# Kernel optimization log

Hardware: AMD Instinct MI355X
Metric: run time of the kernel (lower is better)

Reference implementation:

```python
import jax, jax.numpy as jnp
import numpy as np
import math

B, S, D, H = 2, 2048, 2048, 16
HD = D // H  # 128
EPS = 1e-5


def setup_inputs() -> dict:
    key = jax.random.key(0)
    ks = jax.random.split(key, 8)
    s = 0.02
    return {
        "x": jax.random.normal(ks[0], (B, S, D), jnp.float32),
        "ln1_s": jnp.ones((D,), jnp.float32),
        "ln1_b": jnp.zeros((D,), jnp.float32),
        "Wq": jax.random.normal(ks[1], (D, D), jnp.float32) * s,
        "Wk": jax.random.normal(ks[2], (D, D), jnp.float32) * s,
        "Wv": jax.random.normal(ks[3], (D, D), jnp.float32) * s,
        "Wo": jax.random.normal(ks[4], (D, D), jnp.float32) * s,
        "bo": jnp.zeros((D,), jnp.float32),
        "ln2_s": jnp.ones((D,), jnp.float32),
        "ln2_b": jnp.zeros((D,), jnp.float32),
        "W1": jax.random.normal(ks[5], (D, 4 * D), jnp.float32) * s,
        "b1": jnp.zeros((4 * D,), jnp.float32),
        "W2": jax.random.normal(ks[6], (4 * D, D), jnp.float32) * s,
        "b2": jnp.zeros((D,), jnp.float32),
    }


def _layernorm(x, scale, shift):
    mean = jnp.mean(x, axis=-1, keepdims=True)
    var = jnp.var(x, axis=-1, keepdims=True)  # unbiased=False
    return scale * (x - mean) * jax.lax.rsqrt(var + EPS) + shift


def _gelu_tanh(x):
    c = math.sqrt(2.0 / math.pi)
    return 0.5 * x * (1.0 + jnp.tanh(c * (x + 0.044715 * x * x * x)))


def reference(x, ln1_s, ln1_b, Wq, Wk, Wv, Wo, bo, ln2_s, ln2_b, W1, b1, W2, b2):
    b, n, d = x.shape
    # --- pre-norm MHA ---
    xn = _layernorm(x, ln1_s, ln1_b)
    q = (xn @ Wq).reshape(b, n, H, HD)
    k = (xn @ Wk).reshape(b, n, H, HD)
    v = (xn @ Wv).reshape(b, n, H, HD)
    scores = jnp.einsum("bqhd,bkhd->bhqk", q, k) / math.sqrt(HD)
    causal = jnp.tril(jnp.ones((n, n), bool))  # True = keep
    scores = jnp.where(causal, scores, -jnp.inf)
    attn = jax.nn.softmax(scores, axis=-1)
    ctx = jnp.einsum("bhqk,bkhd->bqhd", attn, v).reshape(b, n, d)
    attn_out = ctx @ Wo + bo
    x = x + attn_out
    # --- pre-norm FFN ---
    xn2 = _layernorm(x, ln2_s, ln2_b)
    h = _gelu_tanh(xn2 @ W1 + b1)
    ff_out = h @ W2 + b2
    return x + ff_out
```

## Files before the change

kernel.cpp:

```cpp
#include <hip/hip_runtime.h>

typedef unsigned short u16;
typedef __attribute__((ext_vector_type(8))) short short8;
typedef __attribute__((ext_vector_type(8))) __bf16 bf16x8;
typedef __attribute__((ext_vector_type(4))) float f32x4;

#define DEV __device__ __forceinline__

DEV float bf2f(u16 u) {
    union { unsigned v; float f; } x; x.v = ((unsigned)u) << 16; return x.f;
}
DEV u16 f2bf(float f) {
    union { float f; unsigned v; } x; x.f = f;
    unsigned r = x.v + 0x7fff + ((x.v >> 16) & 1);
    return (u16)(r >> 16);
}

DEV f32x4 mfma16(short8 a, short8 b, f32x4 c) {
    return __builtin_amdgcn_mfma_f32_16x16x32_bf16(
        __builtin_bit_cast(bf16x8, a), __builtin_bit_cast(bf16x8, b), c, 0, 0, 0);
}

typedef const __attribute__((address_space(1))) void* gas_ptr;
typedef __attribute__((address_space(3))) void* las_ptr;

__global__ __launch_bounds__(256) void transpose_kernel(
    const float* __restrict__ in, u16* __restrict__ out, int R, int C)
{
    __shared__ u16 t[64][65];
    int tid = threadIdx.x;
    int bc = blockIdx.x * 64, br = blockIdx.y * 64;
    int r = tid >> 2, cs = (tid & 3) * 16;
    const float* ip = in + (size_t)(br + r) * C + bc + cs;
    f32x4 v0 = *(const f32x4*)ip, v1 = *(const f32x4*)(ip + 4),
          v2 = *(const f32x4*)(ip + 8), v3 = *(const f32x4*)(ip + 12);
#pragma unroll
    for (int j = 0; j < 4; j++) {
        t[r][cs + j]      = f2bf(v0[j]);
        t[r][cs + 4 + j]  = f2bf(v1[j]);
        t[r][cs + 8 + j]  = f2bf(v2[j]);
        t[r][cs + 12 + j] = f2bf(v3[j]);
    }
    __syncthreads();
    int n = tid >> 2, ks = (tid & 3) * 16;
    short8 o0, o1;
#pragma unroll
    for (int j = 0; j < 8; j++) { o0[j] = (short)t[ks + j][n]; o1[j] = (short)t[ks + 8 + j][n]; }
    u16* op = out + (size_t)(bc + n) * R + br + ks;
    *(short8*)op = o0;
    *(short8*)(op + 8) = o1;
}

template<int INBF>
__global__ __launch_bounds__(256) void ln_kernel(
    const void* __restrict__ xp, const float* __restrict__ sc, const float* __restrict__ sh,
    u16* __restrict__ out)
{
    int row = blockIdx.x, tid = threadIdx.x;
    float f[8], sum = 0.f, ss = 0.f;
    if (INBF) {
        short8 v = *(const short8*)((const u16*)xp + (size_t)row * 2048 + tid * 8);
#pragma unroll
        for (int j = 0; j < 8; j++) f[j] = bf2f((u16)v[j]);
    } else {
        const f32x4* xr = (const f32x4*)((const float*)xp + (size_t)row * 2048 + tid * 8);
        f32x4 a = xr[0], b = xr[1];
#pragma unroll
        for (int j = 0; j < 4; j++) { f[j] = a[j]; f[4 + j] = b[j]; }
    }
#pragma unroll
    for (int j = 0; j < 8; j++) { sum += f[j]; ss += f[j] * f[j]; }
#pragma unroll
    for (int m = 1; m < 64; m <<= 1) { sum += __shfl_xor(sum, m, 64); ss += __shfl_xor(ss, m, 64); }
    __shared__ float red[8];
    int w = tid >> 6, l = tid & 63;
    if (l == 0) { red[w] = sum; red[4 + w] = ss; }
    __syncthreads();
    sum = red[0] + red[1] + red[2] + red[3];
    ss  = red[4] + red[5] + red[6] + red[7];
    float mean = sum * (1.f / 2048.f);
    float var  = ss * (1.f / 2048.f) - mean * mean;
    float rstd = rsqrtf(var + 1e-5f);
    const f32x4* sp = (const f32x4*)(sc + tid * 8);
    const f32x4* bp = (const f32x4*)(sh + tid * 8);
    f32x4 s0 = sp[0], s1 = sp[1], b0 = bp[0], b1 = bp[1];
    short8 o;
#pragma unroll
    for (int j = 0; j < 4; j++) {
        o[j]     = (short)f2bf((f[j] - mean) * rstd * s0[j] + b0[j]);
        o[4 + j] = (short)f2bf((f[4 + j] - mean) * rstd * s1[j] + b1[j]);
    }
    *(short8*)(out + (size_t)row * 2048 + tid * 8) = o;
}

template<int EPI, int OUTF, int RESBF, int SPLITM, int SHAREB>
__global__ __launch_bounds__(256, 2) void gemm_bt2(
    const u16* __restrict__ A, const u16* __restrict__ BT, void* __restrict__ Cp,
    const float* __restrict__ bias, const void* __restrict__ res, int M, int N, int K)
{
    __shared__ u16 As[2][128 * 64];
    __shared__ u16 Bs[2][128 * 64];
    int tid = threadIdx.x, l = tid & 63, w = tid >> 6;

    int nbx = gridDim.x, nby = gridDim.y;
    int nwg = nbx * nby;
    int orig = blockIdx.y * nbx + blockIdx.x;
    int nch = nwg >> 3;
    int wg = (orig & 7) * nch + (orig >> 3);
    int bx, by;
    if (SHAREB) { bx = wg / nby; by = wg % nby; }
    else        { by = wg / nbx; bx = wg % nbx; }

    int mbase = by * 128, nbase = bx * 128;
    const u16* Ag = A + (size_t)mbase * K;
    const u16* Bg = BT + (size_t)nbase * K;
    int NT = K >> 6;

    auto stage = [&](const u16* G, u16* Ld, int t) {
#pragma unroll
        for (int g = 0; g < 4; g++) {
            int ci = g * 256 + tid;
            int r = ci >> 3, chp = ci & 7;
            int ch = chp ^ (r & 7);
            const u16* gp = G + (size_t)r * K + t * 64 + ch * 8;
            __builtin_amdgcn_global_load_lds((gas_ptr)gp, (las_ptr)(Ld + (g * 256 + w * 64) * 8), 16, 0, 0);
        }
    };

    f32x4 acc[4][4];
#pragma unroll
    for (int i = 0; i < 4; i++)
#pragma unroll
        for (int j = 0; j < 4; j++) acc[i][j] = (f32x4){0.f, 0.f, 0.f, 0.f};
    int wr = (w >> 1) * 64, wc = (w & 1) * 64;

    stage(Ag, As[0], 0); stage(Bg, Bs[0], 0);
    __syncthreads();
    int buf = 0;
    for (int t = 0; t < NT; ++t) {
        if (t + 1 < NT) { stage(Ag, As[buf ^ 1], t + 1); stage(Bg, Bs[buf ^ 1], t + 1); }
        short8 af[2][4], bfr[2][4];
#pragma unroll
        for (int ks = 0; ks < 2; ks++) {
            int c = ks * 4 + (l >> 4);
#pragma unroll
            for (int i = 0; i < 4; i++) {
                int ra = wr + i * 16 + (l & 15);
                af[ks][i] = *(const short8*)&As[buf][ra * 64 + ((c ^ (ra & 7)) << 3)];
                int rb = wc + i * 16 + (l & 15);
                bfr[ks][i] = *(const short8*)&Bs[buf][rb * 64 + ((c ^ (rb & 7)) << 3)];
            }
        }
        __builtin_amdgcn_s_setprio(1);
#pragma unroll
        for (int ks = 0; ks < 2; ks++)
#pragma unroll
            for (int mi = 0; mi < 4; mi++)
#pragma unroll
                for (int ni = 0; ni < 4; ni++)
                    acc[mi][ni] = mfma16(af[ks][mi], bfr[ks][ni], acc[mi][ni]);
        __builtin_amdgcn_s_setprio(0);
        __syncthreads();
        buf ^= 1;
    }

#pragma unroll
    for (int mi = 0; mi < 4; mi++) {
#pragma unroll
        for (int ni = 0; ni < 4; ni++) {
            int col = nbase + wc + ni * 16 + (l & 15);
            float bval = (EPI != 0) ? bias[col] : 0.f;
#pragma unroll
            for (int r = 0; r < 4; r++) {
                int row = mbase + wr + mi * 16 + (l >> 4) * 4 + r;
                float v = acc[mi][ni][r];
                if (EPI == 1) {
                    size_t ridx = (size_t)row * N + col;
                    float rv = RESBF ? bf2f(((const u16*)res)[ridx]) : ((const float*)res)[ridx];
                    v += bval + rv;
                }
                if (EPI == 2) {
                    v += bval;
                    float tt = tanhf(0.7978845608028654f * (v + 0.044715f * v * v * v));
                    v = 0.5f * v * (1.f + tt);
                }
                if (SPLITM == 1) {
                    ((u16*)Cp)[(size_t)(col >> 11) * 8388608ULL + (size_t)row * 2048 + (col & 2047)] = f2bf(v);
                } else if (SPLITM == 2) {
                    ((u16*)Cp)[(size_t)(col >> 11) * 4194304ULL + (size_t)row * 2048 + (col & 2047)] = f2bf(v);
                } else if (OUTF) {
                    ((float*)Cp)[(size_t)row * N + col] = v;
                } else {
                    ((u16*)Cp)[(size_t)row * N + col] = f2bf(v);
                }
            }
        }
    }
}

__global__ __launch_bounds__(256, 2) void attn_kernel(
    const u16* __restrict__ Q, const u16* __restrict__ Kp, const u16* __restrict__ VTg,
    u16* __restrict__ O)
{
    __shared__ u16 Ks[64 * 128];
    __shared__ u16 VT[128 * 64];
    __shared__ u16 Ps[4 * 2048];
    int tid = threadIdx.x, l = tid & 63, w = tid >> 6;
    int qtl = (int)gridDim.x - 1 - (int)blockIdx.x;
    int bh = blockIdx.y, b = bh >> 4, h = bh & 15;
    const float SCALE = 0.08838834764831845f;
    int qbase = qtl * 128;
    size_t bS = (size_t)b * 2048;
    const u16* vrow = VTg + (size_t)bh * 128 * 2048;

    short8 qf[2][4];
#pragma unroll
    for (int mg = 0; mg < 2; mg++) {
        int qrow = qbase + w * 32 + mg * 16 + (l & 15);
        const u16* qp = Q + (bS + qrow) * 2048 + h * 128 + (l >> 4) * 8;
#pragma unroll
        for (int ds = 0; ds < 4; ds++) qf[mg][ds] = *(const short8*)(qp + ds * 32);
    }
    float m_[2][4], l_[2][4];
    f32x4 o_[2][8];
#pragma unroll
    for (int mg = 0; mg < 2; mg++)
#pragma unroll
        for (int r = 0; r < 4; r++) { m_[mg][r] = -1e30f; l_[mg][r] = 0.f; }
#pragma unroll
    for (int mg = 0; mg < 2; mg++)
#pragma unroll
        for (int d = 0; d < 8; d++) o_[mg][d] = (f32x4){0.f, 0.f, 0.f, 0.f};

    int ktmax = 2 * qtl + 1;
    for (int kt = 0; kt <= ktmax; ++kt) {
        int kbase = kt * 64;
#pragma unroll
        for (int it = 0; it < 4; ++it) {
            int slot = it * 256 + tid;
            int key = slot >> 4, dseg = slot & 15;
            short8 kv = *(const short8*)(Kp + (bS + kbase + key) * 2048 + h * 128 + dseg * 8);
            int kidx = ((key * 256 + dseg * 16) ^ ((key & 7) << 4)) >> 1;
            *(short8*)&Ks[kidx] = kv;
            int d = slot >> 3, k8 = slot & 7;
            short8 vv = *(const short8*)(vrow + (size_t)d * 2048 + kbase + k8 * 8);
            int vidx = ((d * 128 + k8 * 16) ^ ((d & 7) << 4)) >> 1;
            *(short8*)&VT[vidx] = vv;
        }
        __syncthreads();

        f32x4 s[2][4];
#pragma unroll
        for (int mg = 0; mg < 2; mg++)
#pragma unroll
            for (int kg = 0; kg < 4; kg++) s[mg][kg] = (f32x4){0.f, 0.f, 0.f, 0.f};
        __builtin_amdgcn_s_setprio(1);
#pragma unroll
        for (int kg = 0; kg < 4; kg++) {
            int key0 = kg * 16 + (l & 15);
#pragma unroll
            for (int ds = 0; ds < 4; ds++) {
                int i0 = ((key0 * 256 + ds * 64 + (l >> 4) * 16) ^ ((key0 & 7) << 4)) >> 1;
                short8 kb = *(const short8*)&Ks[i0];
                s[0][kg] = mfma16(qf[0][ds], kb, s[0][kg]);
                s[1][kg] = mfma16(qf[1][ds], kb, s[1][kg]);
            }
        }
        __builtin_amdgcn_s_setprio(0);

        bool domask = (kbase + 63) > qbase;
        float alpha[2][4];
        u16* Pw = &Ps[w * 2048];
#pragma unroll
        for (int mg = 0; mg < 2; mg++) {
#pragma unroll
            for (int r = 0; r < 4; r++) {
                int qrow = qbase + w * 32 + mg * 16 + (l >> 4) * 4 + r;
                float aa[4];
#pragma unroll
                for (int kg = 0; kg < 4; kg++) {
                    float a = s[mg][kg][r] * SCALE;
                    if (domask && (kbase + kg * 16 + (l & 15)) > qrow) a = -1e30f;
                    aa[kg] = a;
                }
                float mx = fmaxf(fmaxf(aa[0], aa[1]), fmaxf(aa[2], aa[3]));
                mx = fmaxf(mx, __shfl_xor(mx, 1, 64));
                mx = fmaxf(mx, __shfl_xor(mx, 2, 64));
                mx = fmaxf(mx, __shfl_xor(mx, 4, 64));
                mx = fmaxf(mx, __shfl_xor(mx, 8, 64));
                float mn = fmaxf(m_[mg][r], mx);
                float al = __expf(m_[mg][r] - mn);
                m_[mg][r] = mn;
                float p[4], rs = 0.f;
#pragma unroll
                for (int kg = 0; kg < 4; kg++) { p[kg] = __expf(aa[kg] - mn); rs += p[kg]; }
                rs += __shfl_xor(rs, 1, 64);
                rs += __shfl_xor(rs, 2, 64);
                rs += __shfl_xor(rs, 4, 64);
                rs += __shfl_xor(rs, 8, 64);
                l_[mg][r] = l_[mg][r] * al + rs;
                alpha[mg][r] = al;
#pragma unroll
                for (int kg = 0; kg < 4; kg++) {
                    int col = kg * 16 + (l & 15);
                    int lp = ((l >> 4) * 4 + r) | (((col >> 3) & 3) << 4);
                    Pw[(mg * 2 + (col >> 5)) * 512 + lp * 8 + (col & 7)] = f2bf(p[kg]);
                }
            }
        }
#pragma unroll
        for (int mg = 0; mg < 2; mg++)
#pragma unroll
            for (int dblk = 0; dblk < 8; dblk++)
#pragma unroll
                for (int r = 0; r < 4; r++) o_[mg][dblk][r] *= alpha[mg][r];

        __builtin_amdgcn_s_setprio(1);
#pragma unroll
        for (int kk = 0; kk < 2; kk++) {
            short8 pa0 = *(const short8*)&Pw[(0 * 2 + kk) * 512 + l * 8];
            short8 pa1 = *(const short8*)&Pw[(1 * 2 + kk) * 512 + l * 8];
#pragma unroll
            for (int dblk = 0; dblk < 8; dblk++) {
                int d = dblk * 16 + (l & 15);
                int iv = ((d * 128 + kk * 64 + (l >> 4) * 16) ^ ((d & 7) << 4)) >> 1;
                short8 vb = *(const short8*)&VT[iv];
                o_[0][dblk] = mfma16(pa0, vb, o_[0][dblk]);
                o_[1][dblk] = mfma16(pa1, vb, o_[1][dblk]);
            }
        }
        __builtin_amdgcn_s_setprio(0);
        __syncthreads();
    }

#pragma unroll
    for (int mg = 0; mg < 2; mg++) {
#pragma unroll
        for (int dblk = 0; dblk < 8; dblk++) {
#pragma unroll
            for (int r = 0; r < 4; r++) {
                int qrow = qbase + w * 32 + mg * 16 + (l >> 4) * 4 + r;
                float v = o_[mg][dblk][r] / l_[mg][r];
                O[(bS + qrow) * 2048 + h * 128 + dblk * 16 + (l & 15)] = f2bf(v);
            }
        }
    }
}

extern "C" void kernel_launch(void* const* d_in, const int* in_sizes, int n_in,
                              void* d_out, int out_size, void* d_ws, size_t ws_size,
                              hipStream_t stream)
{
    const float* x    = (const float*)d_in[0];
    const float* ln1s = (const float*)d_in[1];
    const float* ln1b = (const float*)d_in[2];
    const float* Wq   = (const float*)d_in[3];
    const float* Wk   = (const float*)d_in[4];
    const float* Wv   = (const float*)d_in[5];
    const float* Wo   = (const float*)d_in[6];
    const float* bo   = (const float*)d_in[7];
    const float* ln2s = (const float*)d_in[8];
    const float* ln2b = (const float*)d_in[9];
    const float* W1   = (const float*)d_in[10];
    const float* b1   = (const float*)d_in[11];
    const float* W2   = (const float*)d_in[12];
    const float* b2   = (const float*)d_in[13];
    float* out = (float*)d_out;
    const size_t ACT = 8388608ULL;

    u16* ws16 = (u16*)d_ws;
    u16* xn   = ws16;
    u16* q    = ws16 + ACT;
    u16* k    = ws16 + 2 * ACT;
    u16* vT   = ws16 + 3 * ACT;
    u16* hbuf = ws16 + 2 * ACT;
    u16* wt   = ws16 + 6 * ACT;
    u16* x2   = q;
    (void)k;

    dim3 blk(256);
    transpose_kernel<<<dim3(32, 32), blk, 0, stream>>>(Wq, wt,                  2048, 2048);
    transpose_kernel<<<dim3(32, 32), blk, 0, stream>>>(Wk, wt + (ACT >> 1),     2048, 2048);
    transpose_kernel<<<dim3(32, 32), blk, 0, stream>>>(Wv, wt + ACT,            2048, 2048);
    transpose_kernel<<<dim3(32, 32), blk, 0, stream>>>(Wo, wt + 3 * (ACT >> 1), 2048, 2048);
    ln_kernel<0><<<4096, blk, 0, stream>>>(x, ln1s, ln1b, xn);
    gemm_bt2<0, 0, 0, 1, 1><<<dim3(32, 32), blk, 0, stream>>>(xn, wt, q, nullptr, nullptr, 4096, 4096, 2048);
    gemm_bt2<0, 0, 0, 2, 1><<<dim3(32, 16), blk, 0, stream>>>(wt + ACT, xn, vT, nullptr, nullptr, 2048, 4096, 2048);
    attn_kernel<<<dim3(16, 32), blk, 0, stream>>>(q, k, vT, xn);
    gemm_bt2<1, 0, 0, 0, 0><<<dim3(16, 32), blk, 0, stream>>>(xn, wt + 3 * (ACT >> 1), x2, bo, x, 4096, 2048, 2048);
    transpose_kernel<<<dim3(128, 32), blk, 0, stream>>>(W1, wt, 2048, 8192);
    ln_kernel<1><<<4096, blk, 0, stream>>>(x2, ln2s, ln2b, xn);
    gemm_bt2<2, 0, 0, 0, 1><<<dim3(64, 32), blk, 0, stream>>>(xn, wt, hbuf, b1, nullptr, 4096, 8192, 2048);
    transpose_kernel<<<dim3(32, 128), blk, 0, stream>>>(W2, wt, 8192, 2048);
    gemm_bt2<1, 1, 1, 0, 0><<<dim3(16, 32), blk, 0, stream>>>(hbuf, wt, out, b2, x2, 4096, 2048, 8192);
}
```

Before: 669.9 us.

## Replace GEMM with 256x256-tile 8-wave ping-pong pipelined kernel

Replaces the 128x128-tile, 4-wave double-buffered GEMM with a 256x256-tile, 512-thread kernel. Each K step is split into four quarter-tile MFMA phases, and the LDS loads for future K steps are interleaved between phases using explicit barriers, sched_barriers and waitcnts. The larger tile raises arithmetic intensity and the finer staging is meant to overlap global loads with MFMA work. The cost is one workgroup per CU, fewer workgroups per GEMM (e.g. 128 for the 2048-wide outputs) and therefore possible wave-quantization losses, plus fragile hand-written synchronization.

```diff
diff --git a/kernel.cpp b/kernel.cpp
--- a/kernel.cpp
+++ b/kernel.cpp
@@ -6,6 +6,7 @@
 typedef __attribute__((ext_vector_type(4))) float f32x4;
 
 #define DEV __device__ __forceinline__
+#define SB() __builtin_amdgcn_sched_barrier(0)
 
 DEV float bf2f(u16 u) {
     union { unsigned v; float f; } x; x.v = ((unsigned)u) << 16; return x.f;
@@ -94,86 +95,153 @@
 }
 
 template<int EPI, int OUTF, int RESBF, int SPLITM, int SHAREB>
-__global__ __launch_bounds__(256, 2) void gemm_bt2(
+__global__ __launch_bounds__(512, 1) void gemm8p(
     const u16* __restrict__ A, const u16* __restrict__ BT, void* __restrict__ Cp,
     const float* __restrict__ bias, const void* __restrict__ res, int M, int N, int K)
 {
-    __shared__ u16 As[2][128 * 64];
-    __shared__ u16 Bs[2][128 * 64];
+    __shared__ u16 As[2][2][128 * 64];
+    __shared__ u16 Bs[2][2][128 * 64];
     int tid = threadIdx.x, l = tid & 63, w = tid >> 6;
+    int wm = w >> 2, wn = w & 3;
 
     int nbx = gridDim.x, nby = gridDim.y;
     int nwg = nbx * nby;
     int orig = blockIdx.y * nbx + blockIdx.x;
-    int nch = nwg >> 3;
-    int wg = (orig & 7) * nch + (orig >> 3);
+    int wg = (orig & 7) * (nwg >> 3) + (orig >> 3);
     int bx, by;
     if (SHAREB) { bx = wg / nby; by = wg % nby; }
     else        { by = wg / nbx; bx = wg % nbx; }
 
-    int mbase = by * 128, nbase = bx * 128;
+    int mbase = by * 256, nbase = bx * 256;
     const u16* Ag = A + (size_t)mbase * K;
     const u16* Bg = BT + (size_t)nbase * K;
     int NT = K >> 6;
 
-    auto stage = [&](const u16* G, u16* Ld, int t) {
-#pragma unroll
-        for (int g = 0; g < 4; g++) {
-            int ci = g * 256 + tid;
-            int r = ci >> 3, chp = ci & 7;
-            int ch = chp ^ (r & 7);
-            const u16* gp = G + (size_t)r * K + t * 64 + ch * 8;
-            __builtin_amdgcn_global_load_lds((gas_ptr)gp, (las_ptr)(Ld + (g * 256 + w * 64) * 8), 16, 0, 0);
+    auto stageA = [&](int b, int h, int tt) {
+#pragma unroll
+        for (int g = 0; g < 2; g++) {
+            int ci = g * 512 + tid;
+            int pr = ci >> 3, chp = ci & 7;
+            int ch = chp ^ (pr & 7);
+            int gr = (pr & 63) + ((pr >> 6) << 7) + h * 64;
+            const u16* gp = Ag + (size_t)gr * K + tt * 64 + ch * 8;
+            __builtin_amdgcn_global_load_lds((gas_ptr)gp,
+                (las_ptr)&As[b][h][(g * 512 + w * 64) * 8], 16, 0, 0);
         }
     };
-
-    f32x4 acc[4][4];
-#pragma unroll
-    for (int i = 0; i < 4; i++)
+    auto stageB = [&](int b, int h, int tt) {
+#pragma unroll
+        for (int g = 0; g < 2; g++) {
+            int ci = g * 512 + tid;
+            int pr = ci >> 3, chp = ci & 7;
+            int ch = chp ^ (pr & 7);
+            int gr = ((pr >> 5) << 6) + (pr & 31) + h * 32;
+            const u16* gp = Bg + (size_t)gr * K + tt * 64 + ch * 8;
+            __builtin_amdgcn_global_load_lds((gas_ptr)gp,
+                (las_ptr)&Bs[b][h][(g * 512 + w * 64) * 8], 16, 0, 0);
+        }
+    };
+    auto readA = [&](int b, int h, int i, int ks) -> short8 {
+        int pr = wm * 64 + i * 16 + (l & 15);
+        int c = (ks * 4 + (l >> 4)) ^ (pr & 7);
+        return *(const short8*)&As[b][h][pr * 64 + c * 8];
+    };
+    auto readB = [&](int b, int h, int j, int ks) -> short8 {
+        int pr = wn * 32 + j * 16 + (l & 15);
+        int c = (ks * 4 + (l >> 4)) ^ (pr & 7);
+        return *(const short8*)&Bs[b][h][pr * 64 + c * 8];
+    };
+
+    f32x4 acc[8][4];
+#pragma unroll
+    for (int i = 0; i < 8; i++)
 #pragma unroll
         for (int j = 0; j < 4; j++) acc[i][j] = (f32x4){0.f, 0.f, 0.f, 0.f};
-    int wr = (w >> 1) * 64, wc = (w & 1) * 64;
-
-    stage(Ag, As[0], 0); stage(Bg, Bs[0], 0);
-    __syncthreads();
-    int buf = 0;
+
+    stageA(0, 0, 0); stageB(0, 0, 0); stageB(0, 1, 0); stageA(0, 1, 0);
+    stageA(1, 0, 1); stageB(1, 1, 1); stageA(1, 1, 1);
+    asm volatile("s_waitcnt vmcnt(6)" ::: "memory");
+    SB(); __builtin_amdgcn_s_barrier(); SB();
+
     for (int t = 0; t < NT; ++t) {
-        if (t + 1 < NT) { stage(Ag, As[buf ^ 1], t + 1); stage(Bg, Bs[buf ^ 1], t + 1); }
-        short8 af[2][4], bfr[2][4];
-#pragma unroll
-        for (int ks = 0; ks < 2; ks++) {
-            int c = ks * 4 + (l >> 4);
-#pragma unroll
-            for (int i = 0; i < 4; i++) {
-                int ra = wr + i * 16 + (l & 15);
-                af[ks][i] = *(const short8*)&As[buf][ra * 64 + ((c ^ (ra & 7)) << 3)];
-                int rb = wc + i * 16 + (l & 15);
-                bfr[ks][i] = *(const short8*)&Bs[buf][rb * 64 + ((c ^ (rb & 7)) << 3)];
-            }
-        }
+        int p = t & 1, q = p ^ 1;
+        short8 a[4][2], bb[2][2];
+#pragma unroll
+        for (int i = 0; i < 4; i++) { a[i][0] = readA(p, 0, i, 0); a[i][1] = readA(p, 0, i, 1); }
+#pragma unroll
+        for (int j = 0; j < 2; j++) { bb[j][0] = readB(p, 0, j, 0); bb[j][1] = readB(p, 0, j, 1); }
+        if (t + 1 < NT) stageB(q, 0, t + 1);
+        SB(); __builtin_amdgcn_s_barrier();
+        asm volatile("s_waitcnt lgkmcnt(0)" ::: "memory"); SB();
         __builtin_amdgcn_s_setprio(1);
 #pragma unroll
         for (int ks = 0; ks < 2; ks++)
 #pragma unroll
-            for (int mi = 0; mi < 4; mi++)
-#pragma unroll
-                for (int ni = 0; ni < 4; ni++)
-                    acc[mi][ni] = mfma16(af[ks][mi], bfr[ks][ni], acc[mi][ni]);
-        __builtin_amdgcn_s_setprio(0);
-        __syncthreads();
-        buf ^= 1;
-    }
-
-#pragma unroll
-    for (int mi = 0; mi < 4; mi++) {
-#pragma unroll
-        for (int ni = 0; ni < 4; ni++) {
-            int col = nbase + wc + ni * 16 + (l & 15);
+            for (int i = 0; i < 4; i++)
+#pragma unroll
+                for (int j = 0; j < 2; j++)
+                    acc[i][j] = mfma16(a[i][ks], bb[j][ks], acc[i][j]);
+        __builtin_amdgcn_s_setprio(0);
+        SB(); __builtin_amdgcn_s_barrier(); SB();
+#pragma unroll
+        for (int j = 0; j < 2; j++) { bb[j][0] = readB(p, 1, j, 0); bb[j][1] = readB(p, 1, j, 1); }
+        if (t + 2 < NT) stageA(p, 0, t + 2);
+        SB(); __builtin_amdgcn_s_barrier();
+        asm volatile("s_waitcnt lgkmcnt(0)" ::: "memory"); SB();
+        __builtin_amdgcn_s_setprio(1);
+#pragma unroll
+        for (int ks = 0; ks < 2; ks++)
+#pragma unroll
+            for (int i = 0; i < 4; i++)
+#pragma unroll
+                for (int j = 0; j < 2; j++)
+                    acc[i][2 + j] = mfma16(a[i][ks], bb[j][ks], acc[i][2 + j]);
+        __builtin_amdgcn_s_setprio(0);
+        SB(); __builtin_amdgcn_s_barrier(); SB();
+#pragma unroll
+        for (int i = 0; i < 4; i++) { a[i][0] = readA(p, 1, i, 0); a[i][1] = readA(p, 1, i, 1); }
+        if (t + 2 < NT) stageB(p, 1, t + 2);
+        SB(); __builtin_amdgcn_s_barrier();
+        asm volatile("s_waitcnt lgkmcnt(0)" ::: "memory"); SB();
+        __builtin_amdgcn_s_setprio(1);
+#pragma unroll
+        for (int ks = 0; ks < 2; ks++)
+#pragma unroll
+            for (int i = 0; i < 4; i++)
+#pragma unroll
+                for (int j = 0; j < 2; j++)
+                    acc[4 + i][2 + j] = mfma16(a[i][ks], bb[j][ks], acc[4 + i][2 + j]);
+        __builtin_amdgcn_s_setprio(0);
+        SB(); __builtin_amdgcn_s_barrier(); SB();
+#pragma unroll
+        for (int j = 0; j < 2; j++) { bb[j][0] = readB(p, 0, j, 0); bb[j][1] = readB(p, 0, j, 1); }
+        if (t + 2 < NT) stageA(p, 1, t + 2);
+        SB(); __builtin_amdgcn_s_barrier();
+        asm volatile("s_waitcnt lgkmcnt(0)" ::: "memory"); SB();
+        __builtin_amdgcn_s_setprio(1);
+#pragma unroll
+        for (int ks = 0; ks < 2; ks++)
+#pragma unroll
+            for (int i = 0; i < 4; i++)
+#pragma unroll
+                for (int j = 0; j < 2; j++)
+                    acc[4 + i][j] = mfma16(a[i][ks], bb[j][ks], acc[4 + i][j]);
+        __builtin_amdgcn_s_setprio(0);
+        if (t + 2 < NT)      { asm volatile("s_waitcnt vmcnt(6)" ::: "memory"); }
+        else if (t + 1 < NT) { asm volatile("s_waitcnt vmcnt(0)" ::: "memory"); }
+        SB(); __builtin_amdgcn_s_barrier(); SB();
+    }
+
+#pragma unroll
+    for (int mf = 0; mf < 8; mf++) {
+#pragma unroll
+        for (int nf = 0; nf < 4; nf++) {
+            int col = nbase + wn * 64 + nf * 16 + (l & 15);
             float bval = (EPI != 0) ? bias[col] : 0.f;
 #pragma unroll
             for (int r = 0; r < 4; r++) {
-                int row = mbase + wr + mi * 16 + (l >> 4) * 4 + r;
-                float v = acc[mi][ni][r];
+                int row = mbase + wm * 128 + mf * 16 + (l >> 4) * 4 + r;
+                float v = acc[mf][nf][r];
                 if (EPI == 1) {
                     size_t ridx = (size_t)row * N + col;
                     float rv = RESBF ? bf2f(((const u16*)res)[ridx]) : ((const float*)res)[ridx];
@@ -378,19 +446,19 @@
     u16* x2   = q;
     (void)k;
 
-    dim3 blk(256);
+    dim3 blk(256), blk8(512);
     transpose_kernel<<<dim3(32, 32), blk, 0, stream>>>(Wq, wt,                  2048, 2048);
     transpose_kernel<<<dim3(32, 32), blk, 0, stream>>>(Wk, wt + (ACT >> 1),     2048, 2048);
     transpose_kernel<<<dim3(32, 32), blk, 0, stream>>>(Wv, wt + ACT,            2048, 2048);
     transpose_kernel<<<dim3(32, 32), blk, 0, stream>>>(Wo, wt + 3 * (ACT >> 1), 2048, 2048);
     ln_kernel<0><<<4096, blk, 0, stream>>>(x, ln1s, ln1b, xn);
-    gemm_bt2<0, 0, 0, 1, 1><<<dim3(32, 32), blk, 0, stream>>>(xn, wt, q, nullptr, nullptr, 4096, 4096, 2048);
-    gemm_bt2<0, 0, 0, 2, 1><<<dim3(32, 16), blk, 0, stream>>>(wt + ACT, xn, vT, nullptr, nullptr, 2048, 4096, 2048);
+    gemm8p<0, 0, 0, 1, 1><<<dim3(16, 16), blk8, 0, stream>>>(xn, wt, q, nullptr, nullptr, 4096, 4096, 2048);
+    gemm8p<0, 0, 0, 2, 1><<<dim3(16, 8), blk8, 0, stream>>>(wt + ACT, xn, vT, nullptr, nullptr, 2048, 4096, 2048);
     attn_kernel<<<dim3(16, 32), blk, 0, stream>>>(q, k, vT, xn);
-    gemm_bt2<1, 0, 0, 0, 0><<<dim3(16, 32), blk, 0, stream>>>(xn, wt + 3 * (ACT >> 1), x2, bo, x, 4096, 2048, 2048);
+    gemm8p<1, 0, 0, 0, 0><<<dim3(8, 16), blk8, 0, stream>>>(xn, wt + 3 * (ACT >> 1), x2, bo, x, 4096, 2048, 2048);
     transpose_kernel<<<dim3(128, 32), blk, 0, stream>>>(W1, wt, 2048, 8192);
     ln_kernel<1><<<4096, blk, 0, stream>>>(x2, ln2s, ln2b, xn);
-    gemm_bt2<2, 0, 0, 0, 1><<<dim3(64, 32), blk, 0, stream>>>(xn, wt, hbuf, b1, nullptr, 4096, 8192, 2048);
+    gemm8p<2, 0, 0, 0, 1><<<dim3(32, 16), blk8, 0, stream>>>(xn, wt, hbuf, b1, nullptr, 4096, 8192, 2048);
     transpose_kernel<<<dim3(32, 128), blk, 0, stream>>>(W2, wt, 8192, 2048);
-    gemm_bt2<1, 1, 1, 0, 0><<<dim3(16, 32), blk, 0, stream>>>(hbuf, wt, out, b2, x2, 4096, 2048, 8192);
-}
+    gemm8p<1, 1, 1, 0, 0><<<dim3(8, 16), blk8, 0, stream>>>(hbuf, wt, out, b2, x2, 4096, 2048, 8192);
+}
```

Result: slower. 783.9 us (+17.0%).

## Use producer-warp triple-buffered GEMM with 256x128 tiles and fuse weight transposes

Applied to the files above, without the earlier changes.

Replaces the double-buffered GEMM with a warp-specialized kernel. A ninth wavefront issues all global-to-LDS loads into a three-slot ring, while eight compute wavefronts run MFMAs on a 256x128 tile. The four square weight transposes are also merged into one launch. This aims to overlap loads with compute and raise reuse per tile, at the cost of one block per CU, a large LDS footprint, and hand-tuned waitcnt/barrier synchronisation that could be fragile.

```diff
diff --git a/kernel.cpp b/kernel.cpp
--- a/kernel.cpp
+++ b/kernel.cpp
@@ -6,6 +6,7 @@
 typedef __attribute__((ext_vector_type(4))) float f32x4;
 
 #define DEV __device__ __forceinline__
+#define SB() __builtin_amdgcn_sched_barrier(0)
 
 DEV float bf2f(u16 u) {
     union { unsigned v; float f; } x; x.v = ((unsigned)u) << 16; return x.f;
@@ -23,6 +24,37 @@
 
 typedef const __attribute__((address_space(1))) void* gas_ptr;
 typedef __attribute__((address_space(3))) void* las_ptr;
+
+__global__ __launch_bounds__(256) void transpose4_kernel(
+    const float* __restrict__ w0, const float* __restrict__ w1,
+    const float* __restrict__ w2, const float* __restrict__ w3,
+    u16* __restrict__ out)
+{
+    __shared__ u16 t[64][65];
+    int tid = threadIdx.x, z = blockIdx.z;
+    const float* in = (z == 0) ? w0 : (z == 1) ? w1 : (z == 2) ? w2 : w3;
+    u16* op0 = out + (size_t)z * 4194304ULL;
+    int bc = blockIdx.x * 64, br = blockIdx.y * 64;
+    int r = tid >> 2, cs = (tid & 3) * 16;
+    const float* ip = in + (size_t)(br + r) * 2048 + bc + cs;
+    f32x4 v0 = *(const f32x4*)ip, v1 = *(const f32x4*)(ip + 4),
+          v2 = *(const f32x4*)(ip + 8), v3 = *(const f32x4*)(ip + 12);
+#pragma unroll
+    for (int j = 0; j < 4; j++) {
+        t[r][cs + j]      = f2bf(v0[j]);
+        t[r][cs + 4 + j]  = f2bf(v1[j]);
+        t[r][cs + 8 + j]  = f2bf(v2[j]);
+        t[r][cs + 12 + j] = f2bf(v3[j]);
+    }
+    __syncthreads();
+    int n = tid >> 2, ks = (tid & 3) * 16;
+    short8 o0, o1;
+#pragma unroll
+    for (int j = 0; j < 8; j++) { o0[j] = (short)t[ks + j][n]; o1[j] = (short)t[ks + 8 + j][n]; }
+    u16* op = op0 + (size_t)(bc + n) * 2048 + br + ks;
+    *(short8*)op = o0;
+    *(short8*)(op + 8) = o1;
+}
 
 __global__ __launch_bounds__(256) void transpose_kernel(
     const float* __restrict__ in, u16* __restrict__ out, int R, int C)
@@ -94,61 +126,87 @@
 }
 
 template<int EPI, int OUTF, int RESBF, int SPLITM, int SHAREB>
-__global__ __launch_bounds__(256, 2) void gemm_bt2(
+__global__ __launch_bounds__(576, 1) void gemm_pc(
     const u16* __restrict__ A, const u16* __restrict__ BT, void* __restrict__ Cp,
     const float* __restrict__ bias, const void* __restrict__ res, int M, int N, int K)
 {
-    __shared__ u16 As[2][128 * 64];
-    __shared__ u16 Bs[2][128 * 64];
+    __shared__ u16 As[3][256 * 64];
+    __shared__ u16 Bs[3][128 * 64];
     int tid = threadIdx.x, l = tid & 63, w = tid >> 6;
 
     int nbx = gridDim.x, nby = gridDim.y;
     int nwg = nbx * nby;
     int orig = blockIdx.y * nbx + blockIdx.x;
-    int nch = nwg >> 3;
-    int wg = (orig & 7) * nch + (orig >> 3);
+    int wg = (orig & 7) * (nwg >> 3) + (orig >> 3);
     int bx, by;
     if (SHAREB) { bx = wg / nby; by = wg % nby; }
     else        { by = wg / nbx; bx = wg % nbx; }
 
-    int mbase = by * 128, nbase = bx * 128;
+    int mbase = by * 256, nbase = bx * 128;
     const u16* Ag = A + (size_t)mbase * K;
     const u16* Bg = BT + (size_t)nbase * K;
     int NT = K >> 6;
 
-    auto stage = [&](const u16* G, u16* Ld, int t) {
-#pragma unroll
-        for (int g = 0; g < 4; g++) {
-            int ci = g * 256 + tid;
-            int r = ci >> 3, chp = ci & 7;
-            int ch = chp ^ (r & 7);
-            const u16* gp = G + (size_t)r * K + t * 64 + ch * 8;
-            __builtin_amdgcn_global_load_lds((gas_ptr)gp, (las_ptr)(Ld + (g * 256 + w * 64) * 8), 16, 0, 0);
-        }
-    };
-
+    if (w == 8) {
+        auto pstage = [&](int s, int tt) {
+#pragma unroll
+            for (int g = 0; g < 32; g++) {
+                int c = g * 64 + l;
+                int r = c >> 3, ch = (c & 7) ^ (r & 7);
+                __builtin_amdgcn_global_load_lds(
+                    (gas_ptr)(Ag + (size_t)r * K + tt * 64 + ch * 8),
+                    (las_ptr)&As[s][g * 512], 16, 0, 0);
+            }
+#pragma unroll
+            for (int g = 0; g < 16; g++) {
+                int c = g * 64 + l;
+                int r = c >> 3, ch = (c & 7) ^ (r & 7);
+                __builtin_amdgcn_global_load_lds(
+                    (gas_ptr)(Bg + (size_t)r * K + tt * 64 + ch * 8),
+                    (las_ptr)&Bs[s][g * 512], 16, 0, 0);
+            }
+        };
+        pstage(0, 0); pstage(1, 1);
+        asm volatile("s_waitcnt vmcnt(48)" ::: "memory");
+        SB();
+        __builtin_amdgcn_s_barrier();
+        SB();
+        for (int t = 0; t < NT; ++t) {
+            if (t + 2 < NT) pstage((t + 2) % 3, t + 2);
+            if (t + 1 < NT) {
+                if (t + 2 < NT) { asm volatile("s_waitcnt vmcnt(48)" ::: "memory"); }
+                else            { asm volatile("s_waitcnt vmcnt(0)"  ::: "memory"); }
+            }
+            SB();
+            __builtin_amdgcn_s_barrier();
+            SB();
+        }
+        return;
+    }
+
+    int wm = w >> 1, wn = w & 1;
     f32x4 acc[4][4];
 #pragma unroll
     for (int i = 0; i < 4; i++)
 #pragma unroll
         for (int j = 0; j < 4; j++) acc[i][j] = (f32x4){0.f, 0.f, 0.f, 0.f};
-    int wr = (w >> 1) * 64, wc = (w & 1) * 64;
-
-    stage(Ag, As[0], 0); stage(Bg, Bs[0], 0);
-    __syncthreads();
-    int buf = 0;
+
+    __builtin_amdgcn_s_barrier();
+    SB();
+    int slot = 0;
     for (int t = 0; t < NT; ++t) {
-        if (t + 1 < NT) { stage(Ag, As[buf ^ 1], t + 1); stage(Bg, Bs[buf ^ 1], t + 1); }
+        const u16* Ab = &As[slot][0];
+        const u16* Bb = &Bs[slot][0];
         short8 af[2][4], bfr[2][4];
 #pragma unroll
         for (int ks = 0; ks < 2; ks++) {
             int c = ks * 4 + (l >> 4);
 #pragma unroll
             for (int i = 0; i < 4; i++) {
-                int ra = wr + i * 16 + (l & 15);
-                af[ks][i] = *(const short8*)&As[buf][ra * 64 + ((c ^ (ra & 7)) << 3)];
-                int rb = wc + i * 16 + (l & 15);
-                bfr[ks][i] = *(const short8*)&Bs[buf][rb * 64 + ((c ^ (rb & 7)) << 3)];
+                int ra = wm * 64 + i * 16 + (l & 15);
+                af[ks][i] = *(const short8*)&Ab[ra * 64 + ((c ^ (ra & 7)) << 3)];
+                int rb = wn * 64 + i * 16 + (l & 15);
+                bfr[ks][i] = *(const short8*)&Bb[rb * 64 + ((c ^ (rb & 7)) << 3)];
             }
         }
         __builtin_amdgcn_s_setprio(1);
@@ -160,19 +218,21 @@
                 for (int ni = 0; ni < 4; ni++)
                     acc[mi][ni] = mfma16(af[ks][mi], bfr[ks][ni], acc[mi][ni]);
         __builtin_amdgcn_s_setprio(0);
-        __syncthreads();
-        buf ^= 1;
+        SB();
+        __builtin_amdgcn_s_barrier();
+        SB();
+        slot = (slot == 2) ? 0 : slot + 1;
     }
 
 #pragma unroll
     for (int mi = 0; mi < 4; mi++) {
 #pragma unroll
         for (int ni = 0; ni < 4; ni++) {
-            int col = nbase + wc + ni * 16 + (l & 15);
+            int col = nbase + wn * 64 + ni * 16 + (l & 15);
             float bval = (EPI != 0) ? bias[col] : 0.f;
 #pragma unroll
             for (int r = 0; r < 4; r++) {
-                int row = mbase + wr + mi * 16 + (l >> 4) * 4 + r;
+                int row = mbase + wm * 64 + mi * 16 + (l >> 4) * 4 + r;
                 float v = acc[mi][ni][r];
                 if (EPI == 1) {
                     size_t ridx = (size_t)row * N + col;
@@ -378,19 +438,16 @@
     u16* x2   = q;
     (void)k;
 
-    dim3 blk(256);
-    transpose_kernel<<<dim3(32, 32), blk, 0, stream>>>(Wq, wt,                  2048, 2048);
-    transpose_kernel<<<dim3(32, 32), blk, 0, stream>>>(Wk, wt + (ACT >> 1),     2048, 2048);
-    transpose_kernel<<<dim3(32, 32), blk, 0, stream>>>(Wv, wt + ACT,            2048, 2048);
-    transpose_kernel<<<dim3(32, 32), blk, 0, stream>>>(Wo, wt + 3 * (ACT >> 1), 2048, 2048);
+    dim3 blk(256), blkp(576);
+    transpose4_kernel<<<dim3(32, 32, 4), blk, 0, stream>>>(Wq, Wk, Wv, Wo, wt);
     ln_kernel<0><<<4096, blk, 0, stream>>>(x, ln1s, ln1b, xn);
-    gemm_bt2<0, 0, 0, 1, 1><<<dim3(32, 32), blk, 0, stream>>>(xn, wt, q, nullptr, nullptr, 4096, 4096, 2048);
-    gemm_bt2<0, 0, 0, 2, 1><<<dim3(32, 16), blk, 0, stream>>>(wt + ACT, xn, vT, nullptr, nullptr, 2048, 4096, 2048);
+    gemm_pc<0, 0, 0, 1, 1><<<dim3(32, 16), blkp, 0, stream>>>(xn, wt, q, nullptr, nullptr, 4096, 4096, 2048);
+    gemm_pc<0, 0, 0, 2, 1><<<dim3(32, 8), blkp, 0, stream>>>(wt + ACT, xn, vT, nullptr, nullptr, 2048, 4096, 2048);
     attn_kernel<<<dim3(16, 32), blk, 0, stream>>>(q, k, vT, xn);
-    gemm_bt2<1, 0, 0, 0, 0><<<dim3(16, 32), blk, 0, stream>>>(xn, wt + 3 * (ACT >> 1), x2, bo, x, 4096, 2048, 2048);
+    gemm_pc<1, 0, 0, 0, 0><<<dim3(16, 16), blkp, 0, stream>>>(xn, wt + 3 * (ACT >> 1), x2, bo, x, 4096, 2048, 2048);
     transpose_kernel<<<dim3(128, 32), blk, 0, stream>>>(W1, wt, 2048, 8192);
     ln_kernel<1><<<4096, blk, 0, stream>>>(x2, ln2s, ln2b, xn);
-    gemm_bt2<2, 0, 0, 0, 1><<<dim3(64, 32), blk, 0, stream>>>(xn, wt, hbuf, b1, nullptr, 4096, 8192, 2048);
+    gemm_pc<2, 0, 0, 0, 1><<<dim3(64, 16), blkp, 0, stream>>>(xn, wt, hbuf, b1, nullptr, 4096, 8192, 2048);
     transpose_kernel<<<dim3(32, 128), blk, 0, stream>>>(W2, wt, 8192, 2048);
-    gemm_bt2<1, 1, 1, 0, 0><<<dim3(16, 32), blk, 0, stream>>>(hbuf, wt, out, b2, x2, 4096, 2048, 8192);
-}
+    gemm_pc<1, 1, 1, 0, 0><<<dim3(16, 16), blkp, 0, stream>>>(hbuf, wt, out, b2, x2, 4096, 2048, 8192);
+}
```

New measurement: 619.0 us. 7.6% less time.
